# Performance work log

Measured on AMD Instinct MI355X. Metric: run time of the kernel, lower is better.

The kernel has to match this reference:

```python
import jax, jax.numpy as jnp
import numpy as np
import math

B, N, D = 64, 128, 128          # graphs, nodes per graph, d_model
D_STATE = 2                     # Mamba default d_state
D_CONV = 4                      # Mamba default conv kernel
DT_RANK = math.ceil(D / 16)     # 8
CUTOFF = 10.0
N_GAUSS = 50                    # GaussianSmearing(0, 10, 50)
EPS_RMS = 1e-5


def setup_inputs() -> dict:
    key = jax.random.key(0)
    ks = jax.random.split(key, 12)
    s = 0.05
    inp = {}
    inp['x'] = jax.random.normal(ks[0], (B * N, D), jnp.float32)
    inp['pos'] = jax.random.normal(ks[1], (B * N, 3), jnp.float32) * 5.0
    inp['map_idx'] = jax.random.randint(ks[2], (B * N,), 0, 16)
    inp['batch'] = jnp.repeat(jnp.arange(B), N)
    # RMSNorm
    inp['norm_w'] = jnp.ones((D,), jnp.float32)
    # simple message-passing gnn (stand-in for injected gnn module)
    inp['gnn_w1'] = jax.random.normal(ks[3], (D, D), jnp.float32) * s
    inp['gnn_b1'] = jnp.zeros((D,), jnp.float32)
    inp['gnn_w2'] = jax.random.normal(ks[4], (D, D), jnp.float32) * s
    inp['gnn_b2'] = jnp.zeros((D,), jnp.float32)
    # Linear(50, 1) on Gaussian-smeared edge distances
    inp['lin_w'] = jax.random.normal(ks[5], (N_GAUSS, 1), jnp.float32) * s
    inp['lin_b'] = jnp.zeros((1,), jnp.float32)
    # MambaBlock params (stored [in, out])
    inp['in_proj_w'] = jax.random.normal(ks[6], (D, 2 * D), jnp.float32) * s
    inp['conv_w'] = jax.random.normal(ks[7], (D, D_CONV), jnp.float32) * s
    inp['conv_b'] = jnp.zeros((D,), jnp.float32)
    inp['x_proj_w'] = jax.random.normal(ks[8], (D, DT_RANK + 2 * D_STATE), jnp.float32) * s
    inp['dt_proj_w'] = jax.random.normal(ks[9], (DT_RANK, D), jnp.float32) * s
    inp['dt_proj_b'] = jnp.zeros((D,), jnp.float32)
    inp['A_log'] = jnp.log(jnp.tile(jnp.arange(1, D_STATE + 1, dtype=jnp.float32), (D, 1)))
    inp['D_param'] = jnp.ones((D,), jnp.float32)
    inp['out_proj_w'] = jax.random.normal(ks[10], (D, D), jnp.float32) * s
    return inp


def _rmsnorm(x, w):
    return x * jax.lax.rsqrt(jnp.mean(x * x, axis=-1, keepdims=True) + EPS_RMS) * w


def _mamba(x_t, adj, in_proj_w, conv_w, conv_b, x_proj_w, dt_proj_w, dt_proj_b,
           A_log, D_param, out_proj_w):
    # x_t: [N, D] node sequence for one graph; adj: [N, N] dense edge-value matrix
    L = x_t.shape[0]
    A = -jnp.exp(A_log)                                   # [D, S]
    xr = x_t @ in_proj_w                                  # [L, 2D]
    xm, res = xr[:, :D], xr[:, D:]
    # causal depthwise conv1d (padding d_conv-1, truncated to L)
    xp = jnp.pad(xm, ((D_CONV - 1, 0), (0, 0)))
    xc = conv_b + sum(xp[j:j + L] * conv_w[:, j] for j in range(D_CONV))
    xc = jax.nn.silu(xc)                                  # [L, D]
    dbl = xc @ x_proj_w                                   # [L, dt_rank + 2S]
    delta = dbl[:, :DT_RANK]
    Bm = dbl[:, DT_RANK:DT_RANK + D_STATE]                # [L, S]
    Cm = dbl[:, DT_RANK + D_STATE:]                       # [L, S]
    delta = jax.nn.softplus(delta @ dt_proj_w + dt_proj_b)  # [L, D]
    # temp_adj_padded: ones [D, D] with adjacency slice in top-left
    m = min(L, D)
    adj_pad = jnp.ones((D, D), dtype=adj.dtype).at[:m, :m].set(adj[:m, :m])
    delta_p = delta @ adj_pad                             # [L, D]
    dA = jnp.exp(delta_p[:, :, None] * A[None])           # [L, D, S]
    dBu = delta_p[:, :, None] * Bm[:, None, :] * xc[:, :, None]

    def step(h, t):
        dA_t, dBu_t, C_t = t
        h = dA_t * h + dBu_t                              # [D, S]
        return h, h @ C_t                                 # [D]

    _, ys = jax.lax.scan(step, jnp.zeros((D, D_STATE), x_t.dtype), (dA, dBu, Cm))
    y = ys + xc * D_param
    y = y * jax.nn.silu(res)
    out = y @ out_proj_w
    return jnp.where(jnp.isfinite(out), out, 0.0)


def reference(x, pos, map_idx, batch, norm_w, gnn_w1, gnn_b1, gnn_w2, gnn_b2,
              lin_w, lin_b, in_proj_w, conv_w, conv_b, x_proj_w, dt_proj_w,
              dt_proj_b, A_log, D_param, out_proj_w):
    x1 = _rmsnorm(x, norm_w)                              # [B*N, D]
    xg = x1.reshape(B, N, D)
    pg = pos.reshape(B, N, 3)
    # per-graph radius graph (dense): dist + edge mask
    diff = pg[:, :, None, :] - pg[:, None, :, :]          # [B, N, N, 3]
    d2 = jnp.sum(diff * diff, axis=-1)
    eye = jnp.eye(N, dtype=bool)[None]
    dist = jnp.sqrt(jnp.where(eye, 1.0, d2))              # safe sqrt on diag
    edge_mask = (~eye) & (dist < CUTOFF)                  # [B, N, N]
    em = edge_mask.astype(x1.dtype)
    # simple message-passing gnn: mean-aggregate relu(Wx) over radius neighbors
    h = jax.nn.relu(xg @ gnn_w1 + gnn_b1)
    deg = jnp.clip(jnp.sum(em, axis=-1, keepdims=True), 1.0, None)
    agg = jnp.einsum('bij,bjd->bid', em, h) / deg
    x2 = agg @ gnn_w2 + gnn_b2                            # [B, N, D]
    # GaussianSmearing(0, 10, 50) + Linear(50, 1) -> dense edge-value matrix
    offsets = jnp.linspace(0.0, 10.0, N_GAUSS)
    coeff = -0.5 / (offsets[1] - offsets[0]) ** 2
    smear = jnp.exp(coeff * (dist[..., None] - offsets) ** 2)  # [B, N, N, 50]
    d_dense = smear @ lin_w[:, 0] + lin_b[0]
    adj = jnp.where(edge_mask, d_dense, 0.0)              # sparse-to-dense
    # Mamba mixer over each graph's node sequence
    mix = jax.vmap(lambda xt, a: _mamba(xt, a, in_proj_w, conv_w, conv_b,
                                        x_proj_w, dt_proj_w, dt_proj_b,
                                        A_log, D_param, out_proj_w))
    x3 = mix(x2, adj).reshape(B * N, D)
    output = x3 + x1
    return (output, pos, map_idx)
```

## Files before the change

kernel.cpp:

```cpp
#include <hip/hip_runtime.h>
#include <math.h>

#define B_ 64
#define N_ 128
#define D_ 128
#define BN_ 8192
#define NG_ 50
#define CUTOFF_ 10.0f

typedef __attribute__((ext_vector_type(8))) short short8v;
typedef __attribute__((ext_vector_type(4))) float f32x4;
#define MFMA16 __builtin_amdgcn_mfma_f32_16x16x32_bf16

__device__ __forceinline__ float bf2f(unsigned short h) {
    return __builtin_bit_cast(float, ((unsigned int)h) << 16);
}
__device__ __forceinline__ unsigned short f2bf(float f) {
    unsigned int u = __builtin_bit_cast(unsigned int, f);
    return (unsigned short)((u + 0x7FFFu + ((u >> 16) & 1u)) >> 16);
}
__device__ __forceinline__ void splitbf(float x, unsigned short& h, unsigned short& l) {
    h = f2bf(x);
    l = f2bf(x - bf2f(h));
}
__device__ __forceinline__ void gl_lds(const void* g, void* l) {
    __builtin_amdgcn_global_load_lds(
        (const __attribute__((address_space(1))) void*)g,
        (__attribute__((address_space(3))) void*)l, 16, 0, 0);
}

__global__ __launch_bounds__(256) void setup_k(
        const float* __restrict__ x, const float* __restrict__ norm_w,
        const float* __restrict__ pos, const int* __restrict__ mi,
        const float* __restrict__ lin_w, const float* __restrict__ lin_b,
        const float* __restrict__ w1, const float* __restrict__ w2,
        const float* __restrict__ b2, const float* __restrict__ in_proj,
        const float* __restrict__ xpw, const float* __restrict__ dtw,
        const float* __restrict__ out_proj,
        unsigned short* __restrict__ w1Th, unsigned short* __restrict__ w1Tl,
        unsigned short* __restrict__ WdTh, unsigned short* __restrict__ WdTl,
        unsigned short* __restrict__ opTh, unsigned short* __restrict__ opTl,
        unsigned short* __restrict__ WfTh, unsigned short* __restrict__ WfTl,
        float* __restrict__ bfv,
        float* __restrict__ x1f, unsigned short* __restrict__ x1h,
        unsigned short* __restrict__ x1l,
        unsigned short* __restrict__ adjh, unsigned short* __restrict__ adjl,
        unsigned short* __restrict__ emh, float* __restrict__ rdeg,
        float* __restrict__ out) {
    int blk = blockIdx.x, t = threadIdx.x;
    if (blk < 513) {
        if (blk < 128) {
            if (t < 128) {
                unsigned short h, l;
                splitbf(w1[blk * 128 + t], h, l);
                w1Th[t * 128 + blk] = h; w1Tl[t * 128 + blk] = l;
            }
        } else if (blk < 256) {
            int m = blk - 128;
            if (t < 128) {
                float s = 0.0f;
                #pragma unroll
                for (int r = 0; r < 8; r++) s = fmaf(xpw[m * 12 + r], dtw[r * 128 + t], s);
                unsigned short h, l; splitbf(s, h, l);
                WdTh[t * 128 + m] = h; WdTl[t * 128 + m] = l;
            }
        } else if (blk < 384) {
            int k = blk - 256;
            if (t < 128) {
                unsigned short h, l;
                splitbf(out_proj[k * 128 + t], h, l);
                opTh[t * 128 + k] = h; opTl[t * 128 + k] = l;
            }
        } else if (blk < 512) {
            int k = blk - 384;
            float s = 0.0f;
            #pragma unroll 8
            for (int j = 0; j < 128; j++) s = fmaf(w2[k * 128 + j], in_proj[j * 256 + t], s);
            unsigned short h, l; splitbf(s, h, l);
            WfTh[t * 128 + k] = h; WfTl[t * 128 + k] = l;
        } else {
            float s = 0.0f;
            #pragma unroll 8
            for (int j = 0; j < 128; j++) s = fmaf(b2[j], in_proj[j * 256 + t], s);
            bfv[t] = s;
        }
    } else if (blk < 642) {
        int idx = (blk - 513) * 256 + t;
        if (idx < BN_ * 3) out[(size_t)BN_ * D_ + idx] = pos[idx];
        if (idx < BN_) out[(size_t)BN_ * D_ + BN_ * 3 + idx] = (float)mi[idx];
    } else if (blk < 2690) {
        int rblk = blk - 642;
        int wv = t >> 6, ln = t & 63;
        int row = rblk * 4 + wv;
        const float2* xr = reinterpret_cast<const float2*>(x) + (size_t)row * 64;
        float2 v = xr[ln];
        float s = fmaf(v.x, v.x, v.y * v.y);
        #pragma unroll
        for (int o = 32; o > 0; o >>= 1) s += __shfl_down(s, o, 64);
        float tot = __shfl(s, 0, 64);
        float r = rsqrtf(tot * (1.0f / D_) + 1e-5f);
        float2 wv2 = reinterpret_cast<const float2*>(norm_w)[ln];
        float o0 = v.x * r * wv2.x, o1 = v.y * r * wv2.y;
        reinterpret_cast<float2*>(x1f)[(size_t)row * 64 + ln] = make_float2(o0, o1);
        unsigned short h0, l0, h1, l1;
        splitbf(o0, h0, l0); splitbf(o1, h1, l1);
        reinterpret_cast<ushort2*>(x1h)[(size_t)row * 64 + ln] = make_ushort2(h0, h1);
        reinterpret_cast<ushort2*>(x1l)[(size_t)row * 64 + ln] = make_ushort2(l0, l1);
    } else {
        __shared__ float px[N_], py[N_], pz[N_];
        __shared__ float lw[NG_];
        __shared__ int degs[8];
        int ablk = blk - 2690;
        int bx = ablk & 15, b = ablk >> 4;
        if (t < N_) {
            const float* p = pos + (size_t)(b * N_ + t) * 3;
            px[t] = p[0]; py[t] = p[1]; pz[t] = p[2];
        } else if (t - N_ < NG_) {
            lw[t - N_] = lin_w[t - N_];
        }
        if (t >= 248) degs[t - 248] = 0;
        __syncthreads();
        float linb = lin_b[0];
        int j = t & 127;
        int il = t >> 7;
        const float DEL = 10.0f / 49.0f;
        const float COEFF = -0.5f / (DEL * DEL);
        #pragma unroll
        for (int p = 0; p < 4; p++) {
            int i = bx * 8 + p * 2 + il;
            float dx = px[i] - px[j], dy = py[i] - py[j], dz = pz[i] - pz[j];
            float d2 = dx * dx + dy * dy + dz * dz;
            float dist = (i == j) ? 1.0f : sqrtf(d2);
            bool edge = (i != j) && (dist < CUTOFF_);
            float val = 0.0f;
            if (edge) {
                int g0 = (int)ceilf((dist - 1.75f) / DEL); if (g0 < 0) g0 = 0;
                int g1 = (int)floorf((dist + 1.75f) / DEL); if (g1 > NG_ - 1) g1 = NG_ - 1;
                float s = linb;
                for (int g = g0; g <= g1; g++) {
                    float tt = dist - (float)g * DEL;
                    s += lw[g] * expf(COEFF * tt * tt);
                }
                val = s;
            }
            size_t idx = ((size_t)b * N_ + i) * N_ + j;
            unsigned short h, l; splitbf(val, h, l);
            adjh[idx] = h; adjl[idx] = l;
            emh[idx] = edge ? 0x3F80 : 0;
            unsigned long long msk = __ballot(edge);
            if ((t & 63) == 0) atomicAdd(&degs[p * 2 + il], __popcll(msk));
        }
        __syncthreads();
        if (t < 8) {
            int dg = degs[t];
            rdeg[(size_t)b * N_ + bx * 8 + t] = 1.0f / (float)(dg > 0 ? dg : 1);
        }
    }
}

#define AHOFF 0
#define ALOFF 8192
#define BHOFF 16384
#define BLOFF 32768
template <int EPI, bool ALO>
__global__ __launch_bounds__(256, 3) void mgemm_k(
        const unsigned short* __restrict__ Ah, const unsigned short* __restrict__ Al,
        const unsigned short* __restrict__ BTh, const unsigned short* __restrict__ BTl,
        const float* __restrict__ bias, const float* __restrict__ AUX,
        float* __restrict__ Cf, unsigned short* __restrict__ Ch,
        unsigned short* __restrict__ Cl, float* __restrict__ Cf2,
        int cstride, int wbs) {
    extern __shared__ char sm[];
    int tid = threadIdx.x;
    int row_base = blockIdx.x * 32;
    int col_base = blockIdx.y * 64;

    const unsigned short* pBh = BTh;
    const unsigned short* pBl = BTl;
    if (wbs) {
        size_t bo = (size_t)(row_base >> 7) * (size_t)wbs;
        pBh += bo; pBl += bo;
    }

    #pragma unroll
    for (int i = 0; i < 2; i++) {
        int s = tid + i * 256;
        int row = s >> 4, inner = s & 15;
        int gb = (inner * 16) ^ ((row & 7) << 4);
        size_t gsrc = (size_t)(row_base + row) * 256 + gb;
        gl_lds((const char*)Ah + gsrc, sm + AHOFF + s * 16);
        if (ALO) gl_lds((const char*)Al + gsrc, sm + ALOFF + s * 16);
    }
    #pragma unroll
    for (int i = 0; i < 4; i++) {
        int s = tid + i * 256;
        int n = s >> 4, inner = s & 15;
        int gb = (inner * 16) ^ ((n & 7) << 4);
        size_t gsrc = (size_t)(col_base + n) * 256 + gb;
        gl_lds((const char*)pBh + gsrc, sm + BHOFF + s * 16);
        gl_lds((const char*)pBl + gsrc, sm + BLOFF + s * 16);
    }
    __syncthreads();

    int w = tid >> 6, l = tid & 63;
    int rlow = l & 15, kb_lane = (l >> 4) * 16;
    int nB = w * 16 + rlow;
    int nswz = (nB & 7) << 4;
    f32x4 acc[2] = {{0.f, 0.f, 0.f, 0.f}, {0.f, 0.f, 0.f, 0.f}};
    #pragma unroll
    for (int kb = 0; kb < 4; kb++) {
        int kbyte = kb * 64 + kb_lane;
        short8v bh = *(const short8v*)(sm + BHOFF + nB * 256 + (kbyte ^ nswz));
        short8v bl = *(const short8v*)(sm + BLOFF + nB * 256 + (kbyte ^ nswz));
        #pragma unroll
        for (int rf = 0; rf < 2; rf++) {
            int ra = rf * 16 + rlow;
            int aswz = (ra & 7) << 4;
            short8v ah = *(const short8v*)(sm + AHOFF + ra * 256 + (kbyte ^ aswz));
            acc[rf] = MFMA16(ah, bh, acc[rf], 0, 0, 0);
            acc[rf] = MFMA16(ah, bl, acc[rf], 0, 0, 0);
            if (ALO) {
                short8v al_ = *(const short8v*)(sm + ALOFF + ra * 256 + (kbyte ^ aswz));
                acc[rf] = MFMA16(al_, bh, acc[rf], 0, 0, 0);
            }
        }
    }

    int colg = col_base + w * 16 + rlow;
    #pragma unroll
    for (int rf = 0; rf < 2; rf++) {
        int row0 = row_base + rf * 16 + (l >> 4) * 4;
        if (EPI == 1) {
            float b_ = bias[colg];
            unsigned short hh[4], ll[4];
            #pragma unroll
            for (int q = 0; q < 4; q++) {
                float t = fmaxf(acc[rf][q] + b_, 0.0f);
                splitbf(t, hh[q], ll[q]);
            }
            size_t bb = (size_t)(row0 >> 7) * 16384 + (size_t)colg * 128 + (row0 & 127);
            *reinterpret_cast<ushort4*>(Ch + bb) = make_ushort4(hh[0], hh[1], hh[2], hh[3]);
            *reinterpret_cast<ushort4*>(Cl + bb) = make_ushort4(ll[0], ll[1], ll[2], ll[3]);
        } else if (EPI == 7) {
            size_t bb = ((size_t)(row0 >> 7) * 128 + colg) * 128 + (row0 & 127);
            *reinterpret_cast<float4*>(Cf + bb) =
                make_float4(acc[rf][0], acc[rf][1], acc[rf][2], acc[rf][3]);
        } else if (EPI == 6 && colg >= 128) {
            float b_ = bias[colg];
            float v[4];
            #pragma unroll
            for (int q = 0; q < 4; q++) {
                float rs = acc[rf][q] + b_;
                v[q] = rs / (1.0f + expf(-rs));
            }
            size_t bb = ((size_t)(row0 >> 7) * 128 + (colg - 128)) * 128 + (row0 & 127);
            *reinterpret_cast<float4*>(Cf2 + bb) = make_float4(v[0], v[1], v[2], v[3]);
        } else {
            #pragma unroll
            for (int q = 0; q < 4; q++) {
                int row = row0 + q;
                float t = acc[rf][q];
                if (EPI == 2) {
                    t *= AUX[row];
                    unsigned short h, lo; splitbf(t, h, lo);
                    Ch[(size_t)row * 128 + colg] = h;
                    Cl[(size_t)row * 128 + colg] = lo;
                }
                if (EPI == 4) {
                    t += bias[colg];
                    t = fmaxf(t, 0.0f) + log1pf(expf(-fabsf(t)));
                    unsigned short h, lo; splitbf(t, h, lo);
                    Ch[(size_t)row * 128 + colg] = h;
                    Cl[(size_t)row * 128 + colg] = lo;
                }
                if (EPI == 5) {
                    t = isfinite(t) ? t : 0.0f;
                    t += AUX[(size_t)row * 128 + colg];
                    Cf[(size_t)row * cstride + colg] = t;
                }
                if (EPI == 6) {
                    t += bias[colg];
                    Cf[(size_t)row * 128 + colg] = t;
                }
            }
        }
    }
}

__global__ __launch_bounds__(256) void convsm_k(const float* __restrict__ xm,
                                                const float* __restrict__ conv_w,
                                                const float* __restrict__ conv_b,
                                                const float* __restrict__ xpw,
                                                unsigned short* __restrict__ xch,
                                                unsigned short* __restrict__ xcl,
                                                float* __restrict__ xcT,
                                                float* __restrict__ bcT) {
    int tid = threadIdx.x;
    int slot = tid >> 7;
    int d = tid & 127;
    int ln = tid & 63;
    int wv = (tid >> 6) & 1;
    __shared__ float red[2][2][4];
    __shared__ float xcs[4][128];
    float cw[4];
    #pragma unroll
    for (int jj = 0; jj < 4; jj++) cw[jj] = conv_w[d * 4 + jj];
    float cb = conv_b[d];
    float4 wv4 = *reinterpret_cast<const float4*>(xpw + d * 12 + 8);

    #pragma unroll
    for (int it = 0; it < 2; it++) {
        int row = blockIdx.x * 4 + it * 2 + slot;
        int bt = row & 127;
        float accv = cb;
        #pragma unroll
        for (int jj = 0; jj < 4; jj++) {
            int tt = bt + jj - 3;
            if (tt >= 0) accv = fmaf(xm[((size_t)(row + jj - 3)) * 128 + d], cw[jj], accv);
        }
        float xcv = accv / (1.0f + expf(-accv));
        xcs[it * 2 + slot][d] = xcv;
        unsigned short h, lo; splitbf(xcv, h, lo);
        xch[(size_t)row * D_ + d] = h;
        xcl[(size_t)row * D_ + d] = lo;
        float p0 = xcv * wv4.x, p1 = xcv * wv4.y, p2 = xcv * wv4.z, p3 = xcv * wv4.w;
        #pragma unroll
        for (int o = 32; o > 0; o >>= 1) {
            p0 += __shfl_down(p0, o, 64);
            p1 += __shfl_down(p1, o, 64);
            p2 += __shfl_down(p2, o, 64);
            p3 += __shfl_down(p3, o, 64);
        }
        if (ln == 0) {
            red[slot][wv][0] = p0; red[slot][wv][1] = p1;
            red[slot][wv][2] = p2; red[slot][wv][3] = p3;
        }
        __syncthreads();
        if (d < 4) {
            int b = row >> 7;
            bcT[(size_t)b * 512 + d * 128 + (row & 127)] = red[slot][0][d] + red[slot][1][d];
        }
        __syncthreads();
    }
    if (tid < 128) {
        int b = blockIdx.x >> 5;
        int t0 = (blockIdx.x * 4) & 127;
        float4 v = make_float4(xcs[0][tid], xcs[1][tid], xcs[2][tid], xcs[3][tid]);
        *reinterpret_cast<float4*>(xcT + ((size_t)b * 128 + tid) * 128 + t0) = v;
    }
}

__global__ __launch_bounds__(256) void scan_k(const float* __restrict__ dpT,
                                              const float* __restrict__ xcT,
                                              const float* __restrict__ bcT,
                                              const float* __restrict__ resT,
                                              const float* __restrict__ A_log,
                                              const float* __restrict__ Dpar,
                                              unsigned short* __restrict__ yh,
                                              unsigned short* __restrict__ yl) {
    int g = blockIdx.x * 256 + threadIdx.x;
    int b = g >> 7, d = g & 127;
    float a1 = -expf(A_log[d * 2]);
    float a2 = -expf(A_log[d * 2 + 1]);
    float Dp = Dpar[d];
    const float4* dp4 = reinterpret_cast<const float4*>(dpT + ((size_t)b * 128 + d) * 128);
    const float4* xc4 = reinterpret_cast<const float4*>(xcT + ((size_t)b * 128 + d) * 128);
    const float4* rr4 = reinterpret_cast<const float4*>(resT + ((size_t)b * 128 + d) * 128);
    const float4* b04 = reinterpret_cast<const float4*>(bcT + (size_t)b * 512);
    const float4* b14 = b04 + 32;
    const float4* c04 = b04 + 64;
    const float4* c14 = b04 + 96;
    float h1 = 0.0f, h2 = 0.0f;
    size_t ybase = (size_t)b * 16384 + d;
    #pragma unroll 4
    for (int tc = 0; tc < 32; tc++) {
        float4 dp = dp4[tc], xc = xc4[tc], rr = rr4[tc];
        float4 bm0 = b04[tc], bm1 = b14[tc], cm0 = c04[tc], cm1 = c14[tc];
        #pragma unroll
        for (int q = 0; q < 4; q++) {
            float dpv = (q == 0) ? dp.x : (q == 1) ? dp.y : (q == 2) ? dp.z : dp.w;
            float xcv = (q == 0) ? xc.x : (q == 1) ? xc.y : (q == 2) ? xc.z : xc.w;
            float rv  = (q == 0) ? rr.x : (q == 1) ? rr.y : (q == 2) ? rr.z : rr.w;
            float bmv0 = (q == 0) ? bm0.x : (q == 1) ? bm0.y : (q == 2) ? bm0.z : bm0.w;
            float bmv1 = (q == 0) ? bm1.x : (q == 1) ? bm1.y : (q == 2) ? bm1.z : bm1.w;
            float cmv0 = (q == 0) ? cm0.x : (q == 1) ? cm0.y : (q == 2) ? cm0.z : cm0.w;
            float cmv1 = (q == 0) ? cm1.x : (q == 1) ? cm1.y : (q == 2) ? cm1.z : cm1.w;
            float e1 = expf(dpv * a1), e2 = expf(dpv * a2);
            float bu = dpv * xcv;
            h1 = fmaf(e1, h1, bu * bmv0);
            h2 = fmaf(e2, h2, bu * bmv1);
            float y = fmaf(h1, cmv0, h2 * cmv1);
            float yv = fmaf(xcv, Dp, y) * rv;
            unsigned short hh, ll; splitbf(yv, hh, ll);
            int t = tc * 4 + q;
            yh[ybase + (size_t)t * 128] = hh;
            yl[ybase + (size_t)t * 128] = ll;
        }
    }
}

extern "C" void kernel_launch(void* const* d_in, const int* in_sizes, int n_in,
                              void* d_out, int out_size, void* d_ws, size_t ws_size,
                              hipStream_t stream) {
    const float* x        = (const float*)d_in[0];
    const float* pos      = (const float*)d_in[1];
    const int*   mi       = (const int*)d_in[2];
    const float* norm_w   = (const float*)d_in[4];
    const float* w1       = (const float*)d_in[5];
    const float* b1       = (const float*)d_in[6];
    const float* w2       = (const float*)d_in[7];
    const float* b2       = (const float*)d_in[8];
    const float* lin_w    = (const float*)d_in[9];
    const float* lin_b    = (const float*)d_in[10];
    const float* in_proj  = (const float*)d_in[11];
    const float* conv_w   = (const float*)d_in[12];
    const float* conv_b   = (const float*)d_in[13];
    const float* xpw      = (const float*)d_in[14];
    const float* dtw      = (const float*)d_in[15];
    const float* dtb      = (const float*)d_in[16];
    const float* A_log    = (const float*)d_in[17];
    const float* Dpar     = (const float*)d_in[18];
    const float* out_proj = (const float*)d_in[19];

    float* out = (float*)d_out;
    char* base = (char*)d_ws;
    const size_t MB = 1u << 20;
    const size_t PL = 1048576;

    float* x1f  = (float*)(base);
    float* xm   = (float*)(base + 4 * MB);
    float* resT = (float*)(base + 8 * MB);
    float* dpT  = (float*)(base + 12 * MB);
    float* xcT  = (float*)(base + 16 * MB);
    float* bcT  = (float*)(base + 20 * MB);
    float* rdeg = (float*)(base + 20 * MB + 131072);

    unsigned short* P = (unsigned short*)(base + 21 * MB);
    unsigned short* x1h  = P +  0 * PL;
    unsigned short* x1l  = P +  1 * PL;
    unsigned short* hTh  = P +  2 * PL;
    unsigned short* hTl  = P +  3 * PL;
    unsigned short* aggh = P +  4 * PL;
    unsigned short* aggl = P +  5 * PL;
    unsigned short* xch  = P +  6 * PL;
    unsigned short* xcl  = P +  7 * PL;
    unsigned short* dlh  = P +  8 * PL;
    unsigned short* dll  = P +  9 * PL;
    unsigned short* yh   = P + 10 * PL;
    unsigned short* yl   = P + 11 * PL;
    unsigned short* adjh = P + 12 * PL;
    unsigned short* adjl = P + 13 * PL;
    unsigned short* emh  = P + 14 * PL;

    unsigned short* W = (unsigned short*)(base + 52 * MB);
    unsigned short* w1Th = W;
    unsigned short* w1Tl = W + 16384;
    unsigned short* WdTh = W + 2 * 16384;
    unsigned short* WdTl = W + 3 * 16384;
    unsigned short* opTh = W + 4 * 16384;
    unsigned short* opTl = W + 5 * 16384;
    unsigned short* WfTh = W + 6 * 16384;
    unsigned short* WfTl = WfTh + 32768;
    float* bfv = (float*)(WfTl + 32768);

    const size_t gsm = 49152;

    setup_k<<<3714, 256, 0, stream>>>(x, norm_w, pos, mi, lin_w, lin_b,
                                      w1, w2, b2, in_proj, xpw, dtw, out_proj,
                                      w1Th, w1Tl, WdTh, WdTl, opTh, opTl, WfTh, WfTl,
                                      bfv, x1f, x1h, x1l, adjh, adjl, emh, rdeg, out);
    mgemm_k<1, true><<<dim3(256, 2), 256, gsm, stream>>>(
        x1h, x1l, w1Th, w1Tl, b1, nullptr, nullptr, hTh, hTl, nullptr, 128, 0);
    mgemm_k<2, false><<<dim3(256, 2), 256, gsm, stream>>>(
        emh, emh, hTh, hTl, nullptr, rdeg, nullptr, aggh, aggl, nullptr, 128, 16384);
    mgemm_k<6, true><<<dim3(256, 4), 256, gsm, stream>>>(
        aggh, aggl, WfTh, WfTl, bfv, nullptr, xm, nullptr, nullptr, resT, 128, 0);
    convsm_k<<<2048, 256, 0, stream>>>(xm, conv_w, conv_b, xpw, xch, xcl, xcT, bcT);
    mgemm_k<4, true><<<dim3(256, 2), 256, gsm, stream>>>(
        xch, xcl, WdTh, WdTl, dtb, nullptr, nullptr, dlh, dll, nullptr, 128, 0);
    mgemm_k<7, true><<<dim3(256, 2), 256, gsm, stream>>>(
        dlh, dll, adjh, adjl, nullptr, nullptr, dpT, nullptr, nullptr, nullptr, 128, 16384);
    scan_k<<<32, 256, 0, stream>>>(dpT, xcT, bcT, resT, A_log, Dpar, yh, yl);
    mgemm_k<5, true><<<dim3(256, 2), 256, gsm, stream>>>(
        yh, yl, opTh, opTl, nullptr, x1f, out, nullptr, nullptr, nullptr, 128, 0);
}
```

Measured before the change: 95.70 us.

## Fuse all stages into one persistent kernel with grid-wide atomic barriers

Replaces the chain of nine kernel launches (setup, six GEMMs, conv, scan) with a single persistent kernel of 512 blocks. Stages are separated by a software grid barrier built on an atomic counter, and the counter is zeroed by a memset before the launch. The aim is to remove launch gaps and per-kernel tail effects. The scan now runs on 64 blocks and stages dp/xc/res tiles through swizzled LDS. The Gaussian smearing loop now uses a recurrence in place of one exp per term. The risks are that co-residency of all 512 blocks must hold or the barrier deadlocks, the scan and conv stages leave most blocks idle, and occupancy is limited to 2 blocks per CU by the static LDS.

```diff
diff --git a/kernel.cpp b/kernel.cpp
--- a/kernel.cpp
+++ b/kernel.cpp
@@ -7,6 +7,7 @@
 #define BN_ 8192
 #define NG_ 50
 #define CUTOFF_ 10.0f
+#define NB_ 512
 
 typedef __attribute__((ext_vector_type(8))) short short8v;
 typedef __attribute__((ext_vector_type(4))) float f32x4;
@@ -29,133 +30,16 @@
         (__attribute__((address_space(3))) void*)l, 16, 0, 0);
 }
 
-__global__ __launch_bounds__(256) void setup_k(
-        const float* __restrict__ x, const float* __restrict__ norm_w,
-        const float* __restrict__ pos, const int* __restrict__ mi,
-        const float* __restrict__ lin_w, const float* __restrict__ lin_b,
-        const float* __restrict__ w1, const float* __restrict__ w2,
-        const float* __restrict__ b2, const float* __restrict__ in_proj,
-        const float* __restrict__ xpw, const float* __restrict__ dtw,
-        const float* __restrict__ out_proj,
-        unsigned short* __restrict__ w1Th, unsigned short* __restrict__ w1Tl,
-        unsigned short* __restrict__ WdTh, unsigned short* __restrict__ WdTl,
-        unsigned short* __restrict__ opTh, unsigned short* __restrict__ opTl,
-        unsigned short* __restrict__ WfTh, unsigned short* __restrict__ WfTl,
-        float* __restrict__ bfv,
-        float* __restrict__ x1f, unsigned short* __restrict__ x1h,
-        unsigned short* __restrict__ x1l,
-        unsigned short* __restrict__ adjh, unsigned short* __restrict__ adjl,
-        unsigned short* __restrict__ emh, float* __restrict__ rdeg,
-        float* __restrict__ out) {
-    int blk = blockIdx.x, t = threadIdx.x;
-    if (blk < 513) {
-        if (blk < 128) {
-            if (t < 128) {
-                unsigned short h, l;
-                splitbf(w1[blk * 128 + t], h, l);
-                w1Th[t * 128 + blk] = h; w1Tl[t * 128 + blk] = l;
-            }
-        } else if (blk < 256) {
-            int m = blk - 128;
-            if (t < 128) {
-                float s = 0.0f;
-                #pragma unroll
-                for (int r = 0; r < 8; r++) s = fmaf(xpw[m * 12 + r], dtw[r * 128 + t], s);
-                unsigned short h, l; splitbf(s, h, l);
-                WdTh[t * 128 + m] = h; WdTl[t * 128 + m] = l;
-            }
-        } else if (blk < 384) {
-            int k = blk - 256;
-            if (t < 128) {
-                unsigned short h, l;
-                splitbf(out_proj[k * 128 + t], h, l);
-                opTh[t * 128 + k] = h; opTl[t * 128 + k] = l;
-            }
-        } else if (blk < 512) {
-            int k = blk - 384;
-            float s = 0.0f;
-            #pragma unroll 8
-            for (int j = 0; j < 128; j++) s = fmaf(w2[k * 128 + j], in_proj[j * 256 + t], s);
-            unsigned short h, l; splitbf(s, h, l);
-            WfTh[t * 128 + k] = h; WfTl[t * 128 + k] = l;
-        } else {
-            float s = 0.0f;
-            #pragma unroll 8
-            for (int j = 0; j < 128; j++) s = fmaf(b2[j], in_proj[j * 256 + t], s);
-            bfv[t] = s;
-        }
-    } else if (blk < 642) {
-        int idx = (blk - 513) * 256 + t;
-        if (idx < BN_ * 3) out[(size_t)BN_ * D_ + idx] = pos[idx];
-        if (idx < BN_) out[(size_t)BN_ * D_ + BN_ * 3 + idx] = (float)mi[idx];
-    } else if (blk < 2690) {
-        int rblk = blk - 642;
-        int wv = t >> 6, ln = t & 63;
-        int row = rblk * 4 + wv;
-        const float2* xr = reinterpret_cast<const float2*>(x) + (size_t)row * 64;
-        float2 v = xr[ln];
-        float s = fmaf(v.x, v.x, v.y * v.y);
-        #pragma unroll
-        for (int o = 32; o > 0; o >>= 1) s += __shfl_down(s, o, 64);
-        float tot = __shfl(s, 0, 64);
-        float r = rsqrtf(tot * (1.0f / D_) + 1e-5f);
-        float2 wv2 = reinterpret_cast<const float2*>(norm_w)[ln];
-        float o0 = v.x * r * wv2.x, o1 = v.y * r * wv2.y;
-        reinterpret_cast<float2*>(x1f)[(size_t)row * 64 + ln] = make_float2(o0, o1);
-        unsigned short h0, l0, h1, l1;
-        splitbf(o0, h0, l0); splitbf(o1, h1, l1);
-        reinterpret_cast<ushort2*>(x1h)[(size_t)row * 64 + ln] = make_ushort2(h0, h1);
-        reinterpret_cast<ushort2*>(x1l)[(size_t)row * 64 + ln] = make_ushort2(l0, l1);
-    } else {
-        __shared__ float px[N_], py[N_], pz[N_];
-        __shared__ float lw[NG_];
-        __shared__ int degs[8];
-        int ablk = blk - 2690;
-        int bx = ablk & 15, b = ablk >> 4;
-        if (t < N_) {
-            const float* p = pos + (size_t)(b * N_ + t) * 3;
-            px[t] = p[0]; py[t] = p[1]; pz[t] = p[2];
-        } else if (t - N_ < NG_) {
-            lw[t - N_] = lin_w[t - N_];
-        }
-        if (t >= 248) degs[t - 248] = 0;
-        __syncthreads();
-        float linb = lin_b[0];
-        int j = t & 127;
-        int il = t >> 7;
-        const float DEL = 10.0f / 49.0f;
-        const float COEFF = -0.5f / (DEL * DEL);
-        #pragma unroll
-        for (int p = 0; p < 4; p++) {
-            int i = bx * 8 + p * 2 + il;
-            float dx = px[i] - px[j], dy = py[i] - py[j], dz = pz[i] - pz[j];
-            float d2 = dx * dx + dy * dy + dz * dz;
-            float dist = (i == j) ? 1.0f : sqrtf(d2);
-            bool edge = (i != j) && (dist < CUTOFF_);
-            float val = 0.0f;
-            if (edge) {
-                int g0 = (int)ceilf((dist - 1.75f) / DEL); if (g0 < 0) g0 = 0;
-                int g1 = (int)floorf((dist + 1.75f) / DEL); if (g1 > NG_ - 1) g1 = NG_ - 1;
-                float s = linb;
-                for (int g = g0; g <= g1; g++) {
-                    float tt = dist - (float)g * DEL;
-                    s += lw[g] * expf(COEFF * tt * tt);
-                }
-                val = s;
-            }
-            size_t idx = ((size_t)b * N_ + i) * N_ + j;
-            unsigned short h, l; splitbf(val, h, l);
-            adjh[idx] = h; adjl[idx] = l;
-            emh[idx] = edge ? 0x3F80 : 0;
-            unsigned long long msk = __ballot(edge);
-            if ((t & 63) == 0) atomicAdd(&degs[p * 2 + il], __popcll(msk));
-        }
-        __syncthreads();
-        if (t < 8) {
-            int dg = degs[t];
-            rdeg[(size_t)b * N_ + bx * 8 + t] = 1.0f / (float)(dg > 0 ? dg : 1);
-        }
-    }
+__device__ __forceinline__ void gbar(unsigned* cnt, unsigned k) {
+    __syncthreads();
+    if (threadIdx.x == 0) {
+        __hip_atomic_fetch_add(cnt, 1u, __ATOMIC_RELEASE, __HIP_MEMORY_SCOPE_AGENT);
+        unsigned target = k * (unsigned)NB_;
+        while (__hip_atomic_load(cnt, __ATOMIC_RELAXED, __HIP_MEMORY_SCOPE_AGENT) < target)
+            __builtin_amdgcn_s_sleep(4);
+        __builtin_amdgcn_fence(__ATOMIC_ACQUIRE, "agent");
+    }
+    __syncthreads();
 }
 
 #define AHOFF 0
@@ -163,25 +47,20 @@
 #define BHOFF 16384
 #define BLOFF 32768
 template <int EPI, bool ALO>
-__global__ __launch_bounds__(256, 3) void mgemm_k(
-        const unsigned short* __restrict__ Ah, const unsigned short* __restrict__ Al,
-        const unsigned short* __restrict__ BTh, const unsigned short* __restrict__ BTl,
-        const float* __restrict__ bias, const float* __restrict__ AUX,
-        float* __restrict__ Cf, unsigned short* __restrict__ Ch,
-        unsigned short* __restrict__ Cl, float* __restrict__ Cf2,
-        int cstride, int wbs) {
-    extern __shared__ char sm[];
+__device__ __forceinline__ void gemm_unit(char* sm, int unit,
+        const unsigned short* Ah, const unsigned short* Al,
+        const unsigned short* BTh, const unsigned short* BTl,
+        const float* bias, const float* AUX,
+        float* Cf, unsigned short* Ch, unsigned short* Cl, float* Cf2, int wbs) {
     int tid = threadIdx.x;
-    int row_base = blockIdx.x * 32;
-    int col_base = blockIdx.y * 64;
-
+    int row_base = (unit & 255) * 32;
+    int col_base = (unit >> 8) * 64;
     const unsigned short* pBh = BTh;
     const unsigned short* pBl = BTl;
     if (wbs) {
         size_t bo = (size_t)(row_base >> 7) * (size_t)wbs;
         pBh += bo; pBl += bo;
     }
-
     #pragma unroll
     for (int i = 0; i < 2; i++) {
         int s = tid + i * 256;
@@ -276,7 +155,7 @@
                 if (EPI == 5) {
                     t = isfinite(t) ? t : 0.0f;
                     t += AUX[(size_t)row * 128 + colg];
-                    Cf[(size_t)row * cstride + colg] = t;
+                    Cf[(size_t)row * 128 + colg] = t;
                 }
                 if (EPI == 6) {
                     t += bias[colg];
@@ -287,30 +166,22 @@
     }
 }
 
-__global__ __launch_bounds__(256) void convsm_k(const float* __restrict__ xm,
-                                                const float* __restrict__ conv_w,
-                                                const float* __restrict__ conv_b,
-                                                const float* __restrict__ xpw,
-                                                unsigned short* __restrict__ xch,
-                                                unsigned short* __restrict__ xcl,
-                                                float* __restrict__ xcT,
-                                                float* __restrict__ bcT) {
+__device__ __forceinline__ void conv_unit(char* smb, int u,
+        const float* xm, const float* conv_w, const float* conv_b,
+        const float* xpw, unsigned short* xch, unsigned short* xcl,
+        float* xcT, float* bcT) {
+    float* redp = (float*)(smb + 49152);
+    float* xcs  = (float*)(smb + 49280);
     int tid = threadIdx.x;
-    int slot = tid >> 7;
-    int d = tid & 127;
-    int ln = tid & 63;
-    int wv = (tid >> 6) & 1;
-    __shared__ float red[2][2][4];
-    __shared__ float xcs[4][128];
+    int slot = tid >> 7, d = tid & 127, ln = tid & 63, wv = (tid >> 6) & 1;
     float cw[4];
     #pragma unroll
     for (int jj = 0; jj < 4; jj++) cw[jj] = conv_w[d * 4 + jj];
     float cb = conv_b[d];
     float4 wv4 = *reinterpret_cast<const float4*>(xpw + d * 12 + 8);
-
     #pragma unroll
     for (int it = 0; it < 2; it++) {
-        int row = blockIdx.x * 4 + it * 2 + slot;
+        int row = u * 4 + it * 2 + slot;
         int bt = row & 127;
         float accv = cb;
         #pragma unroll
@@ -319,7 +190,7 @@
             if (tt >= 0) accv = fmaf(xm[((size_t)(row + jj - 3)) * 128 + d], cw[jj], accv);
         }
         float xcv = accv / (1.0f + expf(-accv));
-        xcs[it * 2 + slot][d] = xcv;
+        xcs[(it * 2 + slot) * 128 + d] = xcv;
         unsigned short h, lo; splitbf(xcv, h, lo);
         xch[(size_t)row * D_ + d] = h;
         xcl[(size_t)row * D_ + d] = lo;
@@ -332,71 +203,280 @@
             p3 += __shfl_down(p3, o, 64);
         }
         if (ln == 0) {
-            red[slot][wv][0] = p0; red[slot][wv][1] = p1;
-            red[slot][wv][2] = p2; red[slot][wv][3] = p3;
+            float* r = redp + (slot * 2 + wv) * 4;
+            r[0] = p0; r[1] = p1; r[2] = p2; r[3] = p3;
         }
         __syncthreads();
         if (d < 4) {
             int b = row >> 7;
-            bcT[(size_t)b * 512 + d * 128 + (row & 127)] = red[slot][0][d] + red[slot][1][d];
+            bcT[(size_t)b * 512 + d * 128 + (row & 127)] =
+                redp[slot * 8 + d] + redp[slot * 8 + 4 + d];
         }
         __syncthreads();
     }
     if (tid < 128) {
-        int b = blockIdx.x >> 5;
-        int t0 = (blockIdx.x * 4) & 127;
-        float4 v = make_float4(xcs[0][tid], xcs[1][tid], xcs[2][tid], xcs[3][tid]);
+        int b = u >> 5;
+        int t0 = (u * 4) & 127;
+        float4 v = make_float4(xcs[tid], xcs[128 + tid], xcs[256 + tid], xcs[384 + tid]);
         *reinterpret_cast<float4*>(xcT + ((size_t)b * 128 + tid) * 128 + t0) = v;
     }
 }
 
-__global__ __launch_bounds__(256) void scan_k(const float* __restrict__ dpT,
-                                              const float* __restrict__ xcT,
-                                              const float* __restrict__ bcT,
-                                              const float* __restrict__ resT,
-                                              const float* __restrict__ A_log,
-                                              const float* __restrict__ Dpar,
-                                              unsigned short* __restrict__ yh,
-                                              unsigned short* __restrict__ yl) {
-    int g = blockIdx.x * 256 + threadIdx.x;
-    int b = g >> 7, d = g & 127;
-    float a1 = -expf(A_log[d * 2]);
-    float a2 = -expf(A_log[d * 2 + 1]);
-    float Dp = Dpar[d];
-    const float4* dp4 = reinterpret_cast<const float4*>(dpT + ((size_t)b * 128 + d) * 128);
-    const float4* xc4 = reinterpret_cast<const float4*>(xcT + ((size_t)b * 128 + d) * 128);
-    const float4* rr4 = reinterpret_cast<const float4*>(resT + ((size_t)b * 128 + d) * 128);
-    const float4* b04 = reinterpret_cast<const float4*>(bcT + (size_t)b * 512);
-    const float4* b14 = b04 + 32;
-    const float4* c04 = b04 + 64;
-    const float4* c14 = b04 + 96;
-    float h1 = 0.0f, h2 = 0.0f;
-    size_t ybase = (size_t)b * 16384 + d;
-    #pragma unroll 4
-    for (int tc = 0; tc < 32; tc++) {
-        float4 dp = dp4[tc], xc = xc4[tc], rr = rr4[tc];
-        float4 bm0 = b04[tc], bm1 = b14[tc], cm0 = c04[tc], cm1 = c14[tc];
-        #pragma unroll
-        for (int q = 0; q < 4; q++) {
-            float dpv = (q == 0) ? dp.x : (q == 1) ? dp.y : (q == 2) ? dp.z : dp.w;
-            float xcv = (q == 0) ? xc.x : (q == 1) ? xc.y : (q == 2) ? xc.z : xc.w;
-            float rv  = (q == 0) ? rr.x : (q == 1) ? rr.y : (q == 2) ? rr.z : rr.w;
-            float bmv0 = (q == 0) ? bm0.x : (q == 1) ? bm0.y : (q == 2) ? bm0.z : bm0.w;
-            float bmv1 = (q == 0) ? bm1.x : (q == 1) ? bm1.y : (q == 2) ? bm1.z : bm1.w;
-            float cmv0 = (q == 0) ? cm0.x : (q == 1) ? cm0.y : (q == 2) ? cm0.z : cm0.w;
-            float cmv1 = (q == 0) ? cm1.x : (q == 1) ? cm1.y : (q == 2) ? cm1.z : cm1.w;
-            float e1 = expf(dpv * a1), e2 = expf(dpv * a2);
-            float bu = dpv * xcv;
-            h1 = fmaf(e1, h1, bu * bmv0);
-            h2 = fmaf(e2, h2, bu * bmv1);
-            float y = fmaf(h1, cmv0, h2 * cmv1);
-            float yv = fmaf(xcv, Dp, y) * rv;
-            unsigned short hh, ll; splitbf(yv, hh, ll);
-            int t = tc * 4 + q;
-            yh[ybase + (size_t)t * 128] = hh;
-            yl[ybase + (size_t)t * 128] = ll;
-        }
-    }
+__global__ __launch_bounds__(256, 2) void mega_k(
+        const float* __restrict__ x, const float* __restrict__ norm_w,
+        const float* __restrict__ pos, const int* __restrict__ mi,
+        const float* __restrict__ lin_w, const float* __restrict__ lin_b,
+        const float* __restrict__ w1, const float* __restrict__ b1,
+        const float* __restrict__ w2, const float* __restrict__ b2,
+        const float* __restrict__ in_proj,
+        const float* __restrict__ conv_w, const float* __restrict__ conv_b,
+        const float* __restrict__ xpw, const float* __restrict__ dtw,
+        const float* __restrict__ dtb,
+        const float* __restrict__ A_log, const float* __restrict__ Dpar,
+        const float* __restrict__ out_proj,
+        unsigned short* __restrict__ w1Th, unsigned short* __restrict__ w1Tl,
+        unsigned short* __restrict__ WdTh, unsigned short* __restrict__ WdTl,
+        unsigned short* __restrict__ opTh, unsigned short* __restrict__ opTl,
+        unsigned short* __restrict__ WfTh, unsigned short* __restrict__ WfTl,
+        float* __restrict__ bfv,
+        float* __restrict__ x1f, unsigned short* __restrict__ x1h,
+        unsigned short* __restrict__ x1l,
+        unsigned short* __restrict__ adjh, unsigned short* __restrict__ adjl,
+        unsigned short* __restrict__ emh, float* __restrict__ rdeg,
+        unsigned short* __restrict__ hTh, unsigned short* __restrict__ hTl,
+        unsigned short* __restrict__ aggh, unsigned short* __restrict__ aggl,
+        float* __restrict__ xm, float* __restrict__ resT,
+        unsigned short* __restrict__ xch, unsigned short* __restrict__ xcl,
+        float* __restrict__ xcT, float* __restrict__ bcT,
+        unsigned short* __restrict__ dlh, unsigned short* __restrict__ dll,
+        float* __restrict__ dpT,
+        unsigned short* __restrict__ yh, unsigned short* __restrict__ yl,
+        unsigned* __restrict__ cnt, float* __restrict__ out) {
+    __shared__ __align__(16) char smb[52224];
+    int blk = blockIdx.x, t = threadIdx.x;
+
+    {
+        float* px = (float*)smb;
+        float* py = px + 128;
+        float* pz = py + 128;
+        float* lw = pz + 128;
+        int* degs = (int*)(lw + 64);
+        for (int ui = 0; ui < 8; ui++) {
+            int u = blk + ui * NB_;
+            if (u >= 3714) continue;
+            if (u < 513) {
+                if (u < 128) {
+                    if (t < 128) {
+                        unsigned short h, l;
+                        splitbf(w1[u * 128 + t], h, l);
+                        w1Th[t * 128 + u] = h; w1Tl[t * 128 + u] = l;
+                    }
+                } else if (u < 256) {
+                    int m = u - 128;
+                    if (t < 128) {
+                        float s = 0.0f;
+                        #pragma unroll
+                        for (int r = 0; r < 8; r++)
+                            s = fmaf(xpw[m * 12 + r], dtw[r * 128 + t], s);
+                        unsigned short h, l; splitbf(s, h, l);
+                        WdTh[t * 128 + m] = h; WdTl[t * 128 + m] = l;
+                    }
+                } else if (u < 384) {
+                    int k = u - 256;
+                    if (t < 128) {
+                        unsigned short h, l;
+                        splitbf(out_proj[k * 128 + t], h, l);
+                        opTh[t * 128 + k] = h; opTl[t * 128 + k] = l;
+                    }
+                } else if (u < 512) {
+                    int k = u - 384;
+                    float s = 0.0f;
+                    #pragma unroll 8
+                    for (int j = 0; j < 128; j++)
+                        s = fmaf(w2[k * 128 + j], in_proj[j * 256 + t], s);
+                    unsigned short h, l; splitbf(s, h, l);
+                    WfTh[t * 128 + k] = h; WfTl[t * 128 + k] = l;
+                } else {
+                    float s = 0.0f;
+                    #pragma unroll 8
+                    for (int j = 0; j < 128; j++)
+                        s = fmaf(b2[j], in_proj[j * 256 + t], s);
+                    bfv[t] = s;
+                }
+            } else if (u < 642) {
+                int idx = (u - 513) * 256 + t;
+                if (idx < BN_ * 3) out[(size_t)BN_ * D_ + idx] = pos[idx];
+                if (idx < BN_) out[(size_t)BN_ * D_ + BN_ * 3 + idx] = (float)mi[idx];
+            } else if (u < 2690) {
+                int rblk = u - 642;
+                int wvv = t >> 6, ln = t & 63;
+                int row = rblk * 4 + wvv;
+                const float2* xr = reinterpret_cast<const float2*>(x) + (size_t)row * 64;
+                float2 v = xr[ln];
+                float s = fmaf(v.x, v.x, v.y * v.y);
+                #pragma unroll
+                for (int o = 32; o > 0; o >>= 1) s += __shfl_down(s, o, 64);
+                float tot = __shfl(s, 0, 64);
+                float r = rsqrtf(tot * (1.0f / D_) + 1e-5f);
+                float2 wv2 = reinterpret_cast<const float2*>(norm_w)[ln];
+                float o0 = v.x * r * wv2.x, o1 = v.y * r * wv2.y;
+                reinterpret_cast<float2*>(x1f)[(size_t)row * 64 + ln] = make_float2(o0, o1);
+                unsigned short h0, l0, h1, l1;
+                splitbf(o0, h0, l0); splitbf(o1, h1, l1);
+                reinterpret_cast<ushort2*>(x1h)[(size_t)row * 64 + ln] = make_ushort2(h0, h1);
+                reinterpret_cast<ushort2*>(x1l)[(size_t)row * 64 + ln] = make_ushort2(l0, l1);
+            } else {
+                int ablk = u - 2690;
+                int bx = ablk & 15, b = ablk >> 4;
+                __syncthreads();
+                if (t < N_) {
+                    const float* p = pos + (size_t)(b * N_ + t) * 3;
+                    px[t] = p[0]; py[t] = p[1]; pz[t] = p[2];
+                } else if (t - N_ < NG_) {
+                    lw[t - N_] = lin_w[t - N_];
+                }
+                if (t >= 248) degs[t - 248] = 0;
+                __syncthreads();
+                float linb = lin_b[0];
+                int j = t & 127;
+                int il = t >> 7;
+                const float DEL = 10.0f / 49.0f;
+                const float COEFF = -0.5f / (DEL * DEL);
+                #pragma unroll
+                for (int p = 0; p < 4; p++) {
+                    int i = bx * 8 + p * 2 + il;
+                    float dx = px[i] - px[j], dy = py[i] - py[j], dz = pz[i] - pz[j];
+                    float d2 = dx * dx + dy * dy + dz * dz;
+                    float dist = (i == j) ? 1.0f : sqrtf(d2);
+                    bool edge = (i != j) && (dist < CUTOFF_);
+                    float val = 0.0f;
+                    if (edge) {
+                        int g0 = (int)ceilf((dist - 1.75f) / DEL); if (g0 < 0) g0 = 0;
+                        int g1 = (int)floorf((dist + 1.75f) / DEL); if (g1 > NG_ - 1) g1 = NG_ - 1;
+                        float dm = dist - (float)g0 * DEL;
+                        float tg = expf(COEFF * dm * dm);
+                        float ug = expf(COEFF * DEL * (DEL - 2.0f * dm));
+                        float s = linb;
+                        for (int g = g0; g <= g1; g++) {
+                            s = fmaf(lw[g], tg, s);
+                            tg *= ug;
+                            ug *= 0.36787944117144233f;
+                        }
+                        val = s;
+                    }
+                    size_t idx = ((size_t)b * N_ + i) * N_ + j;
+                    unsigned short h, l; splitbf(val, h, l);
+                    adjh[idx] = h; adjl[idx] = l;
+                    emh[idx] = edge ? 0x3F80 : 0;
+                    unsigned long long msk = __ballot(edge);
+                    if ((t & 63) == 0) atomicAdd(&degs[p * 2 + il], __popcll(msk));
+                }
+                __syncthreads();
+                if (t < 8) {
+                    int dg = degs[t];
+                    rdeg[(size_t)b * N_ + bx * 8 + t] = 1.0f / (float)(dg > 0 ? dg : 1);
+                }
+            }
+        }
+    }
+    gbar(cnt, 1);
+
+    gemm_unit<1, true>(smb, blk, x1h, x1l, w1Th, w1Tl, b1, nullptr,
+                       nullptr, hTh, hTl, nullptr, 0);
+    gbar(cnt, 2);
+
+    gemm_unit<2, false>(smb, blk, emh, emh, hTh, hTl, nullptr, rdeg,
+                        nullptr, aggh, aggl, nullptr, 16384);
+    gbar(cnt, 3);
+
+    for (int i = 0; i < 2; i++) {
+        __syncthreads();
+        gemm_unit<6, true>(smb, blk + i * NB_, aggh, aggl, WfTh, WfTl, bfv,
+                           nullptr, xm, nullptr, nullptr, resT, 0);
+    }
+    gbar(cnt, 4);
+
+    for (int i = 0; i < 4; i++) {
+        __syncthreads();
+        conv_unit(smb, blk + i * NB_, xm, conv_w, conv_b, xpw, xch, xcl, xcT, bcT);
+    }
+    gbar(cnt, 5);
+
+    gemm_unit<4, true>(smb, blk, xch, xcl, WdTh, WdTl, dtb, nullptr,
+                       nullptr, dlh, dll, nullptr, 0);
+    gbar(cnt, 6);
+
+    gemm_unit<7, true>(smb, blk, dlh, dll, adjh, adjl, nullptr, nullptr,
+                       dpT, nullptr, nullptr, nullptr, 16384);
+    gbar(cnt, 7);
+
+    if (blk < B_) {
+        float* lds = (float*)smb;
+        float* bcl = (float*)(smb + 49152);
+        int b = blk;
+        if (t < 128) {
+            float4 v = reinterpret_cast<const float4*>(bcT + (size_t)b * 512)[t];
+            *reinterpret_cast<float4*>(bcl + t * 4) = v;
+        }
+        float a1 = 0.f, a2 = 0.f, Dp = 0.f;
+        if (t < 128) {
+            a1 = -expf(A_log[t * 2]);
+            a2 = -expf(A_log[t * 2 + 1]);
+            Dp = Dpar[t];
+        }
+        float h1 = 0.0f, h2 = 0.0f;
+        const float4* dp4 = reinterpret_cast<const float4*>(dpT + (size_t)b * 16384);
+        const float4* xc4 = reinterpret_cast<const float4*>(xcT + (size_t)b * 16384);
+        const float4* rr4 = reinterpret_cast<const float4*>(resT + (size_t)b * 16384);
+        size_t ybase = (size_t)b * 16384 + t;
+        for (int c = 0; c < 4; c++) {
+            __syncthreads();
+            #pragma unroll
+            for (int k = 0; k < 4; k++) {
+                int q = t + k * 256;
+                int dd = q >> 3, tq = q & 7;
+                int gidx = dd * 32 + c * 8 + tq;
+                float4 vd = dp4[gidx], vx = xc4[gidx], vr = rr4[gidx];
+                #pragma unroll
+                for (int j = 0; j < 4; j++) {
+                    int tp = tq * 4 + j;
+                    int sw = dd ^ tp;
+                    float fd = (j == 0) ? vd.x : (j == 1) ? vd.y : (j == 2) ? vd.z : vd.w;
+                    float fx = (j == 0) ? vx.x : (j == 1) ? vx.y : (j == 2) ? vx.z : vx.w;
+                    float fr = (j == 0) ? vr.x : (j == 1) ? vr.y : (j == 2) ? vr.z : vr.w;
+                    lds[tp * 128 + sw] = fd;
+                    lds[4096 + tp * 128 + sw] = fx;
+                    lds[8192 + tp * 128 + sw] = fr;
+                }
+            }
+            __syncthreads();
+            if (t < 128) {
+                #pragma unroll 8
+                for (int tp = 0; tp < 32; tp++) {
+                    int sw = t ^ tp;
+                    float dpv = lds[tp * 128 + sw];
+                    float xcv = lds[4096 + tp * 128 + sw];
+                    float rv  = lds[8192 + tp * 128 + sw];
+                    int tg = c * 32 + tp;
+                    float bm0 = bcl[tg], bm1 = bcl[128 + tg];
+                    float cm0 = bcl[256 + tg], cm1 = bcl[384 + tg];
+                    float e1 = expf(dpv * a1), e2 = expf(dpv * a2);
+                    float bu = dpv * xcv;
+                    h1 = fmaf(e1, h1, bu * bm0);
+                    h2 = fmaf(e2, h2, bu * bm1);
+                    float y = fmaf(h1, cm0, h2 * cm1);
+                    float yv = fmaf(xcv, Dp, y) * rv;
+                    unsigned short hh, ll; splitbf(yv, hh, ll);
+                    yh[ybase + (size_t)tg * 128] = hh;
+                    yl[ybase + (size_t)tg * 128] = ll;
+                }
+            }
+        }
+    }
+    gbar(cnt, 8);
+
+    gemm_unit<5, true>(smb, blk, yh, yl, opTh, opTl, nullptr, x1f,
+                       out, nullptr, nullptr, nullptr, 0);
 }
 
 extern "C" void kernel_launch(void* const* d_in, const int* in_sizes, int n_in,
@@ -462,25 +542,14 @@
     unsigned short* WfTh = W + 6 * 16384;
     unsigned short* WfTl = WfTh + 32768;
     float* bfv = (float*)(WfTl + 32768);
-
-    const size_t gsm = 49152;
-
-    setup_k<<<3714, 256, 0, stream>>>(x, norm_w, pos, mi, lin_w, lin_b,
-                                      w1, w2, b2, in_proj, xpw, dtw, out_proj,
-                                      w1Th, w1Tl, WdTh, WdTl, opTh, opTl, WfTh, WfTl,
-                                      bfv, x1f, x1h, x1l, adjh, adjl, emh, rdeg, out);
-    mgemm_k<1, true><<<dim3(256, 2), 256, gsm, stream>>>(
-        x1h, x1l, w1Th, w1Tl, b1, nullptr, nullptr, hTh, hTl, nullptr, 128, 0);
-    mgemm_k<2, false><<<dim3(256, 2), 256, gsm, stream>>>(
-        emh, emh, hTh, hTl, nullptr, rdeg, nullptr, aggh, aggl, nullptr, 128, 16384);
-    mgemm_k<6, true><<<dim3(256, 4), 256, gsm, stream>>>(
-        aggh, aggl, WfTh, WfTl, bfv, nullptr, xm, nullptr, nullptr, resT, 128, 0);
-    convsm_k<<<2048, 256, 0, stream>>>(xm, conv_w, conv_b, xpw, xch, xcl, xcT, bcT);
-    mgemm_k<4, true><<<dim3(256, 2), 256, gsm, stream>>>(
-        xch, xcl, WdTh, WdTl, dtb, nullptr, nullptr, dlh, dll, nullptr, 128, 0);
-    mgemm_k<7, true><<<dim3(256, 2), 256, gsm, stream>>>(
-        dlh, dll, adjh, adjl, nullptr, nullptr, dpT, nullptr, nullptr, nullptr, 128, 16384);
-    scan_k<<<32, 256, 0, stream>>>(dpT, xcT, bcT, resT, A_log, Dpar, yh, yl);
-    mgemm_k<5, true><<<dim3(256, 2), 256, gsm, stream>>>(
-        yh, yl, opTh, opTl, nullptr, x1f, out, nullptr, nullptr, nullptr, 128, 0);
-}
+    unsigned* cnt = (unsigned*)(base + 52 * MB + 331776);
+
+    (void)hipMemsetAsync((void*)cnt, 0, 64, stream);
+    mega_k<<<NB_, 256, 0, stream>>>(
+        x, norm_w, pos, mi, lin_w, lin_b, w1, b1, w2, b2, in_proj,
+        conv_w, conv_b, xpw, dtw, dtb, A_log, Dpar, out_proj,
+        w1Th, w1Tl, WdTh, WdTl, opTh, opTl, WfTh, WfTl, bfv,
+        x1f, x1h, x1l, adjh, adjl, emh, rdeg,
+        hTh, hTl, aggh, aggl, xm, resT, xch, xcl, xcT, bcT,
+        dlh, dll, dpT, yh, yl, cnt, out);
+}
```

New measurement: 353.8 us. 3.7x slower.
